# Kernel optimization log

Hardware: AMD Instinct MI355X
Metric: run time of the kernel (lower is better)

Reference implementation:

```python
import jax, jax.numpy as jnp
import numpy as np
from jax import lax

WS = 5      # window_size
NH = 8      # num_heads
C = 192     # channels
CPH = (2 * C // 3) // (2 * NH)  # per-head channel dim = 8


def _l2n(x):
    # F.normalize(dim=-1) with eps clamp
    n = jnp.linalg.norm(x, axis=-1, keepdims=True)
    return x / jnp.maximum(n, 1e-12)


def _conv3(x, w, b):
    y = lax.conv_general_dilated(x, w, (1, 1), 'SAME',
                                 dimension_numbers=('NCHW', 'OIHW', 'NCHW'))
    return y + b[None, :, None, None]


def _cpb_bias(cpb_w1, cpb_b1, cpb_w2):
    # relative coords table, Swin-V2 style log-spaced
    rel = np.arange(-(WS - 1), WS, dtype=np.float32)
    tbl = np.stack(np.meshgrid(rel, rel, indexing='ij'), axis=-1)  # (2W-1,2W-1,2)
    tbl = tbl / (WS - 1) * 8.0
    tbl = np.sign(tbl) * np.log2(np.abs(tbl) + 1.0) / np.log2(8.0)
    tbl = jnp.asarray(tbl.reshape(-1, 2))                          # (81,2)
    # relative position index (static int table)
    coords = np.stack(np.meshgrid(np.arange(WS), np.arange(WS), indexing='ij')).reshape(2, -1)
    rc = (coords[:, :, None] - coords[:, None, :]).transpose(1, 2, 0)  # (25,25,2)
    rc[..., 0] += WS - 1
    rc[..., 1] += WS - 1
    rc[..., 0] *= 2 * WS - 1
    idx = rc.sum(-1).reshape(-1)                                    # (625,)
    # cpb MLP: Linear(2,512)+ReLU, Linear(512,NH,no bias)
    h = jax.nn.relu(tbl @ cpb_w1.T + cpb_b1)
    bias_tbl = h @ cpb_w2.T                                         # (81, NH)
    bias = bias_tbl[idx].reshape(WS * WS, WS * WS, NH).transpose(2, 0, 1)
    return 16.0 * jax.nn.sigmoid(bias)                              # (NH,25,25)


def _wa(x, logit_scale, bias):
    # windowed cosine attention; note: scores are K@K^T (faithful to source)
    b, c2, h, w = x.shape
    hb, wb = h // WS, w // WS
    # 'b (kv head c) (h dh) (w dw) -> kv (b h w) head (dh dw) c'
    xr = x.reshape(b, 2, NH, CPH, hb, WS, wb, WS)
    xr = xr.transpose(1, 0, 4, 6, 2, 5, 7, 3).reshape(2, b * hb * wb, NH, WS * WS, CPH)
    k, v = xr[0], xr[1]
    kn = _l2n(k)
    scale = jnp.exp(jnp.minimum(logit_scale, jnp.log(100.0)))       # (NH,1,1)
    atn = jnp.einsum('wnic,wnjc->wnij', kn, kn) * scale + bias[None]
    atn = jax.nn.softmax(atn, axis=-1)
    y = jnp.einsum('wnij,wnjc->wnic', atn, v)                       # (bhw,NH,25,CPH)
    y = y.reshape(b, hb, wb, NH, WS, WS, CPH)
    y = y.transpose(0, 3, 6, 1, 4, 2, 5).reshape(b, NH * CPH, h, w)
    return y


def _forward(x, w_in, b_in, w_out, b_out, logit_scale, lr_logit_scale,
             cpb_w1, cpb_b1, cpb_w2):
    b, c, h, w = x.shape
    xp = _conv3(x, w_in, b_in)                                      # (b, 2c, h, w)
    ch = 2 * c // 3
    x0, x1, x2 = xp[:, :ch], xp[:, ch:2 * ch], xp[:, 2 * ch:]
    bias = _cpb_bias(cpb_w1, cpb_b1, cpb_w2)
    ys = []
    # branch 0: plain window attention
    ys.append(_wa(x0, logit_scale, bias))
    # branch 1: shifted windows (note asymmetric shifts, faithful to torch code)
    x1s = jnp.roll(x1, shift=(-WS // 2, -WS // 2), axis=(2, 3))
    y1 = _wa(x1s, logit_scale, bias)
    y1 = jnp.roll(y1, shift=(WS // 2, WS // 2), axis=(2, 3))
    ys.append(y1)
    # branch 2: long-range axial cosine attention
    xr = x2.reshape(b, 2, NH, CPH, h, w).transpose(1, 0, 4, 2, 5, 3)
    xr = xr.reshape(2, b * h, NH, w, CPH)                           # kv,(b h),head,w,c
    k, v = xr[0], xr[1]
    scale = jnp.exp(jnp.minimum(lr_logit_scale, jnp.log(100.0)))
    kn = _l2n(k)
    atn = jax.nn.softmax(jnp.einsum('bnic,bnjc->bnij', kn, kn) * scale, axis=-1)
    v = jnp.einsum('bnij,bnjc->bnic', atn, v)
    # '(b h) head w c -> (b w) head h c'
    k = k.reshape(b, h, NH, w, CPH).transpose(0, 3, 2, 1, 4).reshape(b * w, NH, h, CPH)
    v = v.reshape(b, h, NH, w, CPH).transpose(0, 3, 2, 1, 4).reshape(b * w, NH, h, CPH)
    kn = _l2n(k)
    atn = jax.nn.softmax(jnp.einsum('bnic,bnjc->bnij', kn, kn) * scale, axis=-1)
    v = jnp.einsum('bnij,bnjc->bnic', atn, v)
    # '(b w) head h c -> b (head c) h w'
    y2 = v.reshape(b, w, NH, h, CPH).transpose(0, 2, 4, 3, 1).reshape(b, NH * CPH, h, w)
    ys.append(y2)
    y = jnp.concatenate(ys, axis=1)                                 # (b, c, h, w)
    return _conv3(y, w_out, b_out)


def setup_inputs() -> dict:
    key = jax.random.key(0)
    ks = jax.random.split(key, 8)
    B, H, W = 2, 160, 160
    s = 0.02
    return {
        'x': jax.random.normal(ks[0], (B, C, H, W), jnp.float32),
        'w_in': jax.random.normal(ks[1], (2 * C, C, 3, 3), jnp.float32) * s,
        'b_in': jnp.zeros((2 * C,), jnp.float32),
        'w_out': jax.random.normal(ks[2], (C, C, 3, 3), jnp.float32) * s,
        'b_out': jnp.zeros((C,), jnp.float32),
        'logit_scale': jnp.log(10.0 * jnp.ones((NH, 1, 1), jnp.float32)),
        'lr_logit_scale': jnp.log(10.0 * jnp.ones((NH, 1, 1), jnp.float32)),
        'cpb_w1': jax.random.normal(ks[3], (512, 2), jnp.float32) * s,
        'cpb_b1': jnp.zeros((512,), jnp.float32),
        'cpb_w2': jax.random.normal(ks[4], (NH, 512), jnp.float32) * s,
    }


def reference(x, w_in, b_in, w_out, b_out, logit_scale, lr_logit_scale,
              cpb_w1, cpb_b1, cpb_w2):
    return _forward(x, w_in, b_in, w_out, b_out, logit_scale, lr_logit_scale,
                    cpb_w1, cpb_b1, cpb_w2)
```

## Files before the change

kernel.cpp:

```cpp
#include <hip/hip_runtime.h>
#include <math.h>


typedef __attribute__((ext_vector_type(8))) short short8;
typedef __attribute__((ext_vector_type(4))) short short4v;
typedef __attribute__((ext_vector_type(4))) float f32x4;

constexpr int Hc = 160, Wc = 160, Bc = 2;
constexpr int HPR = 162;
constexpr int HPW = 164;

__device__ inline unsigned short f2bf(float f) {
  union { float f; unsigned u; } v; v.f = f;
  unsigned r = v.u + 0x7FFF + ((v.u >> 16) & 1);
  return (unsigned short)(r >> 16);
}
__device__ inline float bf2f(unsigned short h) {
  union { unsigned u; float f; } v; v.u = ((unsigned)h) << 16;
  return v.f;
}

__device__ inline void gl16(const void* g, void* l) {
  __builtin_amdgcn_global_load_lds((const __attribute__((address_space(1))) unsigned int*)g,
                                   (__attribute__((address_space(3))) unsigned int*)l, 16, 0, 0);
}

__device__ inline float dot8(f32x4 a0, f32x4 a1, f32x4 b0, f32x4 b1) {
  float d = a0[0] * b0[0];
  d = fmaf(a0[1], b0[1], d); d = fmaf(a0[2], b0[2], d); d = fmaf(a0[3], b0[3], d);
  d = fmaf(a1[0], b1[0], d); d = fmaf(a1[1], b1[1], d);
  d = fmaf(a1[2], b1[2], d); d = fmaf(a1[3], b1[3], d);
  return d;
}

__global__ __launch_bounds__(256)
void prep_kernel(const float* __restrict__ x, unsigned short* __restrict__ xpad,
                 unsigned short* __restrict__ ypad,
                 const float* __restrict__ w_in, unsigned short* __restrict__ wtr1,
                 const float* __restrict__ w_out, unsigned short* __restrict__ wtr2,
                 const float* __restrict__ cw1, const float* __restrict__ cb1,
                 const float* __restrict__ cw2, float* __restrict__ biasf) {
  __shared__ float tile[192][33];
  const int bid = blockIdx.x;
  const int t = threadIdx.x;
  if (bid < 1600) {
    int blk = bid;
    const int w0 = (blk % 5) * 32; blk /= 5;
    const int h = blk % 160;
    const int b = blk / 160;
    for (int i = t; i < 192 * 32; i += 256) {
      int c = i >> 5, w = i & 31;
      tile[c][w] = x[(((size_t)b * 192 + c) * 160 + h) * 160 + w0 + w];
    }
    __syncthreads();
    for (int i = t; i < 32 * 192; i += 256) {
      int w = i / 192, c = i % 192;
      xpad[(((size_t)b * HPR + h + 1) * HPW + w0 + w + 1) * 192 + c] = f2bf(tile[c][w]);
    }
  } else if (bid < 1963) {
    const int NPOS = 968;
    const int total = 2 * 2 * NPOS * 24;
    int idx = (bid - 1600) * 256 + t;
    if (idx >= total) return;
    const int ch = idx % 24; int q = idx / 24;
    const int pos = q % NPOS; q /= NPOS;
    const int b = q & 1; const int buf = q >> 1;
    int row, col;
    if (pos < 328) { row = (pos < 164) ? 0 : 161; col = pos % 164; }
    else { int r = pos - 328; row = 1 + (r >> 2); int cm = r & 3; col = cm == 0 ? 0 : 160 + cm; }
    unsigned short* p = (buf ? ypad : xpad) + (((size_t)b * HPR + row) * HPW + col) * 192 + ch * 8;
    short8 z = {};
    *(short8*)p = z;
  } else if (bid < 2395) {
    const bool first = bid < 2251;
    const int CO = first ? 384 : 192;
    const int NT = CO / 16;
    const float* w = first ? w_in : w_out;
    unsigned short* wtr = first ? wtr1 : wtr2;
    int id = (bid - (first ? 1963 : 2251)) * 256 + t;
    if (id >= CO * 192) return;
    const int co = id / 192, ci = id % 192;
    const int cs = ci >> 5, kh = (ci >> 3) & 3, j = ci & 7;
    const int cotile = co >> 4, cor = co & 15;
    const float* wp = w + (size_t)id * 9;
#pragma unroll
    for (int tap = 0; tap < 9; ++tap)
      wtr[((((size_t)tap * 6 + cs) * NT + cotile) * 64 + kh * 16 + cor) * 8 + j] = f2bf(wp[tap]);
  } else {
    if (t >= 64) return;
    const int e = bid - 2395;
    const int d0 = e / 9, d1 = e % 9;
    const int r0 = d0 - 4, r1 = d1 - 4;
    float t0 = log2f(fabsf((float)r0) * 2.0f + 1.0f) * (1.0f / 3.0f); if (r0 < 0) t0 = -t0;
    float t1 = log2f(fabsf((float)r1) * 2.0f + 1.0f) * (1.0f / 3.0f); if (r1 < 0) t1 = -t1;
    const int lane = t;
    float acc[8];
#pragma unroll
    for (int n = 0; n < 8; ++n) acc[n] = 0.f;
    for (int k = lane; k < 512; k += 64) {
      float hk = fmaf(t0, cw1[k * 2 + 0], fmaf(t1, cw1[k * 2 + 1], cb1[k]));
      hk = fmaxf(hk, 0.f);
#pragma unroll
      for (int n = 0; n < 8; ++n) acc[n] = fmaf(hk, cw2[n * 512 + k], acc[n]);
    }
#pragma unroll
    for (int n = 0; n < 8; ++n) {
#pragma unroll
      for (int off = 32; off > 0; off >>= 1) acc[n] += __shfl_xor(acc[n], off, 64);
    }
    if (lane == 0) {
#pragma unroll
      for (int n = 0; n < 8; ++n)
        biasf[e * 8 + n] = 16.0f / (1.0f + expf(-acc[n]));
    }
  }
}

template<int COUT, int CT, int OUTMODE>
__global__ __launch_bounds__(256, 2)
void conv_mfma(const unsigned short* __restrict__ xin, const unsigned short* __restrict__ wtrA,
               const float* __restrict__ bias, unsigned short* __restrict__ obf,
               unsigned short* __restrict__ xk2k, unsigned short* __restrict__ xk2v,
               float* __restrict__ of32) {
  constexpr int CIN = 192;
  constexpr int R = 6;
  constexpr int TOTAL = R * 84 * 4;
  constexpr int SLAB = R * 84 * 32;
  constexpr int NT = COUT / 16;
  __shared__ unsigned short slab[2 * SLAB];
  const int t = threadIdx.x, lane = t & 63, wid = t >> 6;
  const int bx = blockIdx.x, cog = blockIdx.y, b = blockIdx.z;
  const int ws = bx & 1, hb = bx >> 1;
  const int w0 = ws * 80, h0 = hb * 4;
  const int hr = wid;
  const int l15 = lane & 15, l4 = lane >> 4;
  const int co0 = cog * (CT * 16);

  f32x4 acc[5][CT];
#pragma unroll
  for (int ct = 0; ct < CT; ++ct) {
    f32x4 bi;
#pragma unroll
    for (int r = 0; r < 4; ++r) bi[r] = bias[co0 + ct * 16 + l4 * 4 + r];
#pragma unroll
    for (int mt = 0; mt < 5; ++mt) acc[mt][ct] = bi;
  }

  auto stage = [&](int cs, int bufbase) {
#pragma unroll
    for (int ib0 = 0; ib0 < 8; ++ib0) {
      const int ib = ib0 * 4 + wid;
      const int n = ib * 64 + lane;
      if (n < TOTAL) {
        const int c = n & 3, q = n >> 2;
        const int r = q / 84, wv = q - r * 84;
        const int csrc = c ^ ((wv >> 1) & 3);
        const unsigned short* g = xin +
            (((size_t)b * HPR + h0 + r) * HPW + w0 + wv) * CIN + cs * 32 + csrc * 8;
        gl16(g, &slab[bufbase + ib * 512]);
      }
    }
  };

#define BARRIER_CNT                                                              \
  {                                                                              \
    if constexpr (CT == 4)                                                       \
      asm volatile("s_waitcnt vmcnt(36)\n\ts_barrier" ::: "memory");             \
    else                                                                         \
      asm volatile("s_waitcnt vmcnt(18)\n\ts_barrier" ::: "memory");             \
  }

#define LOADA(a, ky, cs)                                                         \
  {                                                                              \
    _Pragma("unroll")                                                            \
    for (int kx = 0; kx < 3; ++kx) {                                             \
      _Pragma("unroll")                                                          \
      for (int ct = 0; ct < CT; ++ct)                                            \
        a[kx * CT + ct] = *(const short8*)(wtrA +                                \
            ((size_t)(((ky) * 3 + kx) * 6 + (cs)) * NT + cog * CT + ct) * 512 +  \
            lane * 8);                                                           \
    }                                                                            \
  }

#define GROUP(a, ky, bufbase)                                                    \
  {                                                                              \
    const unsigned short* srow = &slab[(bufbase) + (hr + (ky)) * 84 * 32];       \
    _Pragma("unroll")                                                            \
    for (int kx = 0; kx < 3; ++kx) {                                             \
      _Pragma("unroll")                                                          \
      for (int mt = 0; mt < 5; ++mt) {                                           \
        const int wv = mt * 16 + l15 + kx;                                       \
        const int cr = l4 ^ ((wv >> 1) & 3);                                     \
        short8 bf = *(const short8*)(srow + wv * 32 + cr * 8);                   \
        _Pragma("unroll")                                                        \
        for (int ct = 0; ct < CT; ++ct)                                          \
          acc[mt][ct] =                                                          \
              __builtin_amdgcn_mfma_f32_16x16x32_bf16(a[kx * CT + ct], bf,       \
                                                      acc[mt][ct], 0, 0, 0);     \
      }                                                                          \
    }                                                                            \
  }

#define CSBODY(cs, base, nbase, LAST)                                            \
  {                                                                              \
    if (!(LAST)) stage((cs) + 1, nbase);                                         \
    __builtin_amdgcn_s_setprio(1);                                               \
    GROUP(A0f, 0, base);                                                         \
    __builtin_amdgcn_s_setprio(0);                                               \
    if (!(LAST)) LOADA(A0f, 0, (cs) + 1);                                        \
    __builtin_amdgcn_s_setprio(1);                                               \
    GROUP(A1f, 1, base);                                                         \
    __builtin_amdgcn_s_setprio(0);                                               \
    if (!(LAST)) LOADA(A1f, 1, (cs) + 1);                                        \
    __builtin_amdgcn_s_setprio(1);                                               \
    GROUP(A2f, 2, base);                                                         \
    __builtin_amdgcn_s_setprio(0);                                               \
    if (!(LAST)) {                                                               \
      LOADA(A2f, 2, (cs) + 1);                                                   \
      BARRIER_CNT;                                                               \
    }                                                                            \
  }

  short8 A0f[3 * CT], A1f[3 * CT], A2f[3 * CT];
  stage(0, 0);
  LOADA(A0f, 0, 0);
  LOADA(A1f, 1, 0);
  LOADA(A2f, 2, 0);
  BARRIER_CNT;

  CSBODY(0, 0, SLAB, 0);
  CSBODY(1, SLAB, 0, 0);
  CSBODY(2, 0, SLAB, 0);
  CSBODY(3, SLAB, 0, 0);
  CSBODY(4, 0, SLAB, 0);
  CSBODY(5, SLAB, 0, 1);
#undef LOADA
#undef GROUP
#undef CSBODY
#undef BARRIER_CNT

  const int h = h0 + hr;
  if (OUTMODE == 0) {
    if (co0 < 256) {
#pragma unroll
      for (int mt = 0; mt < 5; ++mt) {
        const int w = w0 + mt * 16 + l15;
        unsigned short* dst0 = obf + (((size_t)b * Hc + h) * Wc + w) * 256 + co0 + l4 * 4;
#pragma unroll
        for (int ct = 0; ct < CT; ++ct) {
          short4v s;
#pragma unroll
          for (int r = 0; r < 4; ++r) s[r] = (short)f2bf(acc[mt][ct][r]);
          *(short4v*)(dst0 + ct * 16) = s;
        }
      }
    } else {
      unsigned short* xk2 = (co0 == 256) ? xk2k : xk2v;
#pragma unroll
      for (int mt = 0; mt < 5; ++mt) {
        const int w = w0 + mt * 16 + l15;
#pragma unroll
        for (int ct = 0; ct < CT; ++ct) {
          const int rel = ct * 16 + l4 * 4;
          const int head = rel >> 3, within = rel & 7;
          short4v s;
#pragma unroll
          for (int r = 0; r < 4; ++r) s[r] = (short)f2bf(acc[mt][ct][r]);
          *(short4v*)(xk2 + ((((size_t)b * 8 + head) * 160 + h) * 160 + w) * 8 + within) = s;
        }
      }
    }
  } else {
#pragma unroll
    for (int mt = 0; mt < 5; ++mt) {
      const int w = w0 + mt * 16 + l15;
#pragma unroll
      for (int ct = 0; ct < CT; ++ct)
#pragma unroll
        for (int r = 0; r < 4; ++r) {
          const int co = co0 + ct * 16 + l4 * 4 + r;
          of32[(((size_t)b * COUT + co) * Hc + h) * Wc + w] = acc[mt][ct][r];
        }
    }
  }
}

__global__ __launch_bounds__(256)
void attn1_kernel(const unsigned short* __restrict__ xq, const float* __restrict__ biasf,
                  const float* __restrict__ logit_scale, const float* __restrict__ lrs,
                  const unsigned short* __restrict__ xk2k, const unsigned short* __restrict__ xk2v,
                  unsigned short* __restrict__ ypad, unsigned short* __restrict__ vrow) {
  const int bid = blockIdx.x;
  if (bid < 4096) {
    __shared__ f32x4 kn4[8][25][2];
    __shared__ f32x4 vv4[8][25][2];
    const int t = threadIdx.x;
    const int head = t & 7;
    const int i = t >> 3;
    const int b = bid >> 11;
    const int r = bid & 2047;
    const int variant = r >> 10;
    const int blk = r & 1023;
    const int chan_off = variant ? 128 : 0;
    const int y_ch_off = variant ? 64 : 0;
    const int shift_in = variant ? 3 : 0;
    const int shift_out = variant ? 2 : 0;
    const int wb_i = blk % 32, hb_i = blk / 32;
    const int wi = i / 5, wj = i % 5;
    const int gh = hb_i * 5 + wi, gw = wb_i * 5 + wj;
    const int sh = (gh + shift_in) % Hc, sw = (gw + shift_in) % Wc;

    if (i < 25) {
      const unsigned short* base = xq + (((size_t)b * Hc + sh) * Wc + sw) * 256 + chan_off + head * 8;
      short8 kv = *(const short8*)base;
      short8 vv = *(const short8*)(base + 64);
      float k[8]; float nrm = 0.f;
#pragma unroll
      for (int c = 0; c < 8; ++c) { k[c] = bf2f((unsigned short)kv[c]); nrm = fmaf(k[c], k[c], nrm); }
      const float inv = 1.0f / fmaxf(sqrtf(nrm), 1e-12f);
      f32x4 a0, a1, b0, b1;
#pragma unroll
      for (int c = 0; c < 4; ++c) { a0[c] = k[c] * inv; a1[c] = k[c + 4] * inv; }
#pragma unroll
      for (int c = 0; c < 4; ++c) { b0[c] = bf2f((unsigned short)vv[c]); b1[c] = bf2f((unsigned short)vv[c + 4]); }
      kn4[head][i][0] = a0; kn4[head][i][1] = a1;
      vv4[head][i][0] = b0; vv4[head][i][1] = b1;
    }
    __syncthreads();
    if (i >= 25) return;

    const float scale = expf(fminf(logit_scale[head], 4.6051702f));
    const f32x4 q0 = kn4[head][i][0], q1 = kn4[head][i][1];
    float s[25];
#pragma unroll
    for (int j = 0; j < 25; ++j) {
      const float d = dot8(q0, q1, kn4[head][j][0], kn4[head][j][1]);
      const int d0 = wi - (j / 5) + 4, d1 = wj - (j % 5) + 4;
      s[j] = fmaf(d, scale, biasf[(d0 * 9 + d1) * 8 + head]);
    }
    float m = -1e30f;
#pragma unroll
    for (int j = 0; j < 25; ++j) m = fmaxf(m, s[j]);
    float den = 0.f;
    f32x4 acc0 = {0.f, 0.f, 0.f, 0.f}, acc1 = {0.f, 0.f, 0.f, 0.f};
#pragma unroll
    for (int j = 0; j < 25; ++j) {
      const float p = __expf(s[j] - m);
      den += p;
      acc0 += vv4[head][j][0] * p;
      acc1 += vv4[head][j][1] * p;
    }
    const float rden = 1.0f / den;
    const int oh = (gh + shift_out) % Hc, ow = (gw + shift_out) % Wc;
    short8 o;
#pragma unroll
    for (int c = 0; c < 4; ++c) { o[c] = (short)f2bf(acc0[c] * rden); o[c + 4] = (short)f2bf(acc1[c] * rden); }
    *(short8*)(ypad + (((size_t)b * HPR + oh + 1) * HPW + ow + 1) * 192 + y_ch_off + head * 8) = o;
  } else {
    __shared__ f32x4 kn4[160][2];
    __shared__ f32x4 vv4[160][2];
    int u = bid - 4096;
    const int head = u % 8; u /= 8;
    const int h = u % 160;
    const int b = u / 160;
    const int i = threadIdx.x;

    if (i < 160) {
      const size_t base = ((((size_t)b * 8 + head) * 160 + h) * 160 + i) * 8;
      short8 kv = *(const short8*)(xk2k + base);
      short8 vv = *(const short8*)(xk2v + base);
      float k[8]; float nrm = 0.f;
#pragma unroll
      for (int c = 0; c < 8; ++c) { k[c] = bf2f((unsigned short)kv[c]); nrm = fmaf(k[c], k[c], nrm); }
      const float inv = 1.0f / fmaxf(sqrtf(nrm), 1e-12f);
      f32x4 a0, a1, b0, b1;
#pragma unroll
      for (int c = 0; c < 4; ++c) { a0[c] = k[c] * inv; a1[c] = k[c + 4] * inv; }
#pragma unroll
      for (int c = 0; c < 4; ++c) { b0[c] = bf2f((unsigned short)vv[c]); b1[c] = bf2f((unsigned short)vv[c + 4]); }
      kn4[i][0] = a0; kn4[i][1] = a1;
      vv4[i][0] = b0; vv4[i][1] = b1;
    }
    __syncthreads();
    if (i >= 160) return;

    const float scale = expf(fminf(lrs[head], 4.6051702f));
    const f32x4 q0 = kn4[i][0], q1 = kn4[i][1];
    float den = 0.f;
    f32x4 acc0 = {0.f, 0.f, 0.f, 0.f}, acc1 = {0.f, 0.f, 0.f, 0.f};
    for (int j = 0; j < 160; ++j) {
      const float d = dot8(q0, q1, kn4[j][0], kn4[j][1]);
      const float p = __expf(fmaf(d, scale, -scale));
      den += p;
      acc0 += vv4[j][0] * p;
      acc1 += vv4[j][1] * p;
    }
    const float rden = 1.0f / den;
    short8 o;
#pragma unroll
    for (int c = 0; c < 4; ++c) { o[c] = (short)f2bf(acc0[c] * rden); o[c + 4] = (short)f2bf(acc1[c] * rden); }
    *(short8*)(vrow + ((((size_t)b * 8 + head) * 160 + h) * 160 + i) * 8) = o;
  }
}

__global__ __launch_bounds__(640)
void col_attn_kernel(const unsigned short* __restrict__ xk2k, const float* __restrict__ lrs,
                     const unsigned short* __restrict__ vrow, unsigned short* __restrict__ ypad) {
  __shared__ f32x4 knT[4][161][2];
  __shared__ f32x4 vvT[4][161][2];
  int blk = blockIdx.x;
  const int wg = blk % 40; blk /= 40;
  const int head = blk % 8;
  const int b = blk / 8;
  const int w0 = wg * 4;
  const int t = threadIdx.x;

  {
    const int h = t >> 2, wc = t & 3;
    const size_t base = ((((size_t)b * 8 + head) * 160 + h) * 160 + (w0 + wc)) * 8;
    short8 kv = *(const short8*)(xk2k + base);
    short8 vv = *(const short8*)(vrow + base);
    float k[8]; float nrm = 0.f;
#pragma unroll
    for (int c = 0; c < 8; ++c) { k[c] = bf2f((unsigned short)kv[c]); nrm = fmaf(k[c], k[c], nrm); }
    const float inv = 1.0f / fmaxf(sqrtf(nrm), 1e-12f);
    f32x4 a0, a1, b0, b1;
#pragma unroll
    for (int c = 0; c < 4; ++c) { a0[c] = k[c] * inv; a1[c] = k[c + 4] * inv; }
#pragma unroll
    for (int c = 0; c < 4; ++c) { b0[c] = bf2f((unsigned short)vv[c]); b1[c] = bf2f((unsigned short)vv[c + 4]); }
    knT[wc][h][0] = a0; knT[wc][h][1] = a1;
    vvT[wc][h][0] = b0; vvT[wc][h][1] = b1;
  }
  __syncthreads();

  const int wi = t / 160, i = t % 160;
  const float scale = expf(fminf(lrs[head], 4.6051702f));
  const f32x4 q0 = knT[wi][i][0], q1 = knT[wi][i][1];
  float den = 0.f;
  f32x4 acc0 = {0.f, 0.f, 0.f, 0.f}, acc1 = {0.f, 0.f, 0.f, 0.f};
  for (int j = 0; j < 160; ++j) {
    const float d = dot8(q0, q1, knT[wi][j][0], knT[wi][j][1]);
    const float p = __expf(fmaf(d, scale, -scale));
    den += p;
    acc0 += vvT[wi][j][0] * p;
    acc1 += vvT[wi][j][1] * p;
  }
  const float rden = 1.0f / den;
  short8 o;
#pragma unroll
  for (int c = 0; c < 4; ++c) { o[c] = (short)f2bf(acc0[c] * rden); o[c + 4] = (short)f2bf(acc1[c] * rden); }
  *(short8*)(ypad + (((size_t)b * HPR + i + 1) * HPW + w0 + wi + 1) * 192 + 128 + head * 8) = o;
}

extern "C" void kernel_launch(void* const* d_in, const int* in_sizes, int n_in,
                              void* d_out, int out_size, void* d_ws, size_t ws_size,
                              hipStream_t stream) {
  const float* x     = (const float*)d_in[0];
  const float* w_in  = (const float*)d_in[1];
  const float* b_in  = (const float*)d_in[2];
  const float* w_out = (const float*)d_in[3];
  const float* b_out = (const float*)d_in[4];
  const float* ls    = (const float*)d_in[5];
  const float* lrs   = (const float*)d_in[6];
  const float* cw1   = (const float*)d_in[7];
  const float* cb1   = (const float*)d_in[8];
  const float* cw2   = (const float*)d_in[9];
  float* out = (float*)d_out;

  char* p = (char*)d_ws;
  unsigned short* xpad = (unsigned short*)p;  p += (size_t)Bc * HPR * HPW * 192 * 2;
  unsigned short* ypad = (unsigned short*)p;  p += (size_t)Bc * HPR * HPW * 192 * 2;
  unsigned short* xq   = (unsigned short*)p;  p += (size_t)Bc * Hc * Wc * 256 * 2;
  unsigned short* xk2k = (unsigned short*)p;  p += (size_t)Bc * 8 * Hc * Wc * 8 * 2;
  unsigned short* xk2v = (unsigned short*)p;  p += (size_t)Bc * 8 * Hc * Wc * 8 * 2;
  unsigned short* vrow = (unsigned short*)p;  p += (size_t)Bc * 8 * Hc * Wc * 8 * 2;
  unsigned short* wtr1 = (unsigned short*)p;  p += (size_t)9 * 384 * 192 * 2;
  unsigned short* wtr2 = (unsigned short*)p;  p += (size_t)9 * 192 * 192 * 2;
  float* biasf = (float*)p;

  prep_kernel<<<2476, 256, 0, stream>>>(x, xpad, ypad, w_in, wtr1, w_out, wtr2, cw1, cb1, cw2, biasf);
  conv_mfma<384, 4, 0><<<dim3(80, 6, Bc), 256, 0, stream>>>(xpad, wtr1, b_in, xq, xk2k, xk2v, nullptr);
  attn1_kernel<<<4096 + Bc * 160 * 8, 256, 0, stream>>>(xq, biasf, ls, lrs, xk2k, xk2v, ypad, vrow);
  col_attn_kernel<<<Bc * 8 * 40, 640, 0, stream>>>(xk2k, lrs, vrow, ypad);
  conv_mfma<192, 2, 1><<<dim3(80, 6, Bc), 256, 0, stream>>>(ypad, wtr2, b_out, nullptr, nullptr, nullptr, out);
}
```

Baseline: 235.6 us.

## Split output conv over input channels with atomic accumulation; vectorize xpad stores

The output conv grid doubles along z, and each block handles half of the input-channel slices (3 of 6). Partial sums are combined with float atomicAdd into an output that prep_kernel now zeroes first. Only the first half adds the bias. The aim is to raise occupancy and parallelism for the small 192-channel output conv, paid for with atomics, a zeroing pass over the output, and non-deterministic summation order. Separately, the prep transpose now writes 8 bf16 channels per store.

```diff
diff --git a/kernel.cpp b/kernel.cpp
--- a/kernel.cpp
+++ b/kernel.cpp
@@ -39,7 +39,8 @@
                  const float* __restrict__ w_in, unsigned short* __restrict__ wtr1,
                  const float* __restrict__ w_out, unsigned short* __restrict__ wtr2,
                  const float* __restrict__ cw1, const float* __restrict__ cb1,
-                 const float* __restrict__ cw2, float* __restrict__ biasf) {
+                 const float* __restrict__ cw2, float* __restrict__ biasf,
+                 float* __restrict__ outz) {
   __shared__ float tile[192][33];
   const int bid = blockIdx.x;
   const int t = threadIdx.x;
@@ -53,9 +54,12 @@
       tile[c][w] = x[(((size_t)b * 192 + c) * 160 + h) * 160 + w0 + w];
     }
     __syncthreads();
-    for (int i = t; i < 32 * 192; i += 256) {
-      int w = i / 192, c = i % 192;
-      xpad[(((size_t)b * HPR + h + 1) * HPW + w0 + w + 1) * 192 + c] = f2bf(tile[c][w]);
+    for (int i = t; i < 32 * 24; i += 256) {
+      int w = i / 24, c8 = i % 24;
+      short8 o;
+#pragma unroll
+      for (int k = 0; k < 8; ++k) o[k] = (short)f2bf(tile[c8 * 8 + k][w]);
+      *(short8*)(xpad + (((size_t)b * HPR + h + 1) * HPW + w0 + w + 1) * 192 + c8 * 8) = o;
     }
   } else if (bid < 1963) {
     const int NPOS = 968;
@@ -86,7 +90,7 @@
 #pragma unroll
     for (int tap = 0; tap < 9; ++tap)
       wtr[((((size_t)tap * 6 + cs) * NT + cotile) * 64 + kh * 16 + cor) * 8 + j] = f2bf(wp[tap]);
-  } else {
+  } else if (bid < 2476) {
     if (t >= 64) return;
     const int e = bid - 2395;
     const int d0 = e / 9, d1 = e % 9;
@@ -112,6 +116,12 @@
 #pragma unroll
       for (int n = 0; n < 8; ++n)
         biasf[e * 8 + n] = 16.0f / (1.0f + expf(-acc[n]));
+    }
+  } else {
+    const long chunk = (long)(bid - 2476) * 256 + t;
+    if (chunk < 2457600) {
+      f32x4 z = {0.f, 0.f, 0.f, 0.f};
+      *(f32x4*)(outz + chunk * 4) = z;
     }
   }
 }
@@ -129,7 +139,11 @@
   constexpr int NT = COUT / 16;
   __shared__ unsigned short slab[2 * SLAB];
   const int t = threadIdx.x, lane = t & 63, wid = t >> 6;
-  const int bx = blockIdx.x, cog = blockIdx.y, b = blockIdx.z;
+  const int bx = blockIdx.x, cog = blockIdx.y;
+  const int zz = blockIdx.z;
+  const int b    = (OUTMODE == 2) ? (zz >> 1) : zz;
+  const int half = (OUTMODE == 2) ? (zz & 1) : 0;
+  const int cs0  = half * 3;
   const int ws = bx & 1, hb = bx >> 1;
   const int w0 = ws * 80, h0 = hb * 4;
   const int hr = wid;
@@ -141,7 +155,8 @@
   for (int ct = 0; ct < CT; ++ct) {
     f32x4 bi;
 #pragma unroll
-    for (int r = 0; r < 4; ++r) bi[r] = bias[co0 + ct * 16 + l4 * 4 + r];
+    for (int r = 0; r < 4; ++r)
+      bi[r] = (OUTMODE == 2 && half != 0) ? 0.f : bias[co0 + ct * 16 + l4 * 4 + r];
 #pragma unroll
     for (int mt = 0; mt < 5; ++mt) acc[mt][ct] = bi;
   }
@@ -222,18 +237,24 @@
   }
 
   short8 A0f[3 * CT], A1f[3 * CT], A2f[3 * CT];
-  stage(0, 0);
-  LOADA(A0f, 0, 0);
-  LOADA(A1f, 1, 0);
-  LOADA(A2f, 2, 0);
+  stage(cs0, 0);
+  LOADA(A0f, 0, cs0);
+  LOADA(A1f, 1, cs0);
+  LOADA(A2f, 2, cs0);
   BARRIER_CNT;
 
-  CSBODY(0, 0, SLAB, 0);
-  CSBODY(1, SLAB, 0, 0);
-  CSBODY(2, 0, SLAB, 0);
-  CSBODY(3, SLAB, 0, 0);
-  CSBODY(4, 0, SLAB, 0);
-  CSBODY(5, SLAB, 0, 1);
+  if constexpr (OUTMODE == 2) {
+    CSBODY(cs0 + 0, 0, SLAB, 0);
+    CSBODY(cs0 + 1, SLAB, 0, 0);
+    CSBODY(cs0 + 2, 0, SLAB, 1);
+  } else {
+    CSBODY(0, 0, SLAB, 0);
+    CSBODY(1, SLAB, 0, 0);
+    CSBODY(2, 0, SLAB, 0);
+    CSBODY(3, SLAB, 0, 0);
+    CSBODY(4, 0, SLAB, 0);
+    CSBODY(5, SLAB, 0, 1);
+  }
 #undef LOADA
 #undef GROUP
 #undef CSBODY
@@ -270,7 +291,7 @@
         }
       }
     }
-  } else {
+  } else if (OUTMODE == 1) {
 #pragma unroll
     for (int mt = 0; mt < 5; ++mt) {
       const int w = w0 + mt * 16 + l15;
@@ -280,6 +301,18 @@
         for (int r = 0; r < 4; ++r) {
           const int co = co0 + ct * 16 + l4 * 4 + r;
           of32[(((size_t)b * COUT + co) * Hc + h) * Wc + w] = acc[mt][ct][r];
+        }
+    }
+  } else {
+#pragma unroll
+    for (int mt = 0; mt < 5; ++mt) {
+      const int w = w0 + mt * 16 + l15;
+#pragma unroll
+      for (int ct = 0; ct < CT; ++ct)
+#pragma unroll
+        for (int r = 0; r < 4; ++r) {
+          const int co = co0 + ct * 16 + l4 * 4 + r;
+          atomicAdd(&of32[(((size_t)b * COUT + co) * Hc + h) * Wc + w], acc[mt][ct][r]);
         }
     }
   }
@@ -479,9 +512,10 @@
   unsigned short* wtr2 = (unsigned short*)p;  p += (size_t)9 * 192 * 192 * 2;
   float* biasf = (float*)p;
 
-  prep_kernel<<<2476, 256, 0, stream>>>(x, xpad, ypad, w_in, wtr1, w_out, wtr2, cw1, cb1, cw2, biasf);
+  prep_kernel<<<12076, 256, 0, stream>>>(x, xpad, ypad, w_in, wtr1, w_out, wtr2,
+                                         cw1, cb1, cw2, biasf, out);
   conv_mfma<384, 4, 0><<<dim3(80, 6, Bc), 256, 0, stream>>>(xpad, wtr1, b_in, xq, xk2k, xk2v, nullptr);
   attn1_kernel<<<4096 + Bc * 160 * 8, 256, 0, stream>>>(xq, biasf, ls, lrs, xk2k, xk2v, ypad, vrow);
   col_attn_kernel<<<Bc * 8 * 40, 640, 0, stream>>>(xk2k, lrs, vrow, ypad);
-  conv_mfma<192, 2, 1><<<dim3(80, 6, Bc), 256, 0, stream>>>(ypad, wtr2, b_out, nullptr, nullptr, nullptr, out);
-}
+  conv_mfma<192, 2, 2><<<dim3(80, 6, Bc * 2), 256, 0, stream>>>(ypad, wtr2, b_out, nullptr, nullptr, nullptr, out);
+}
```

New measurement: 276.4 us. 1.17x slower.

## Split conv output channels across two wave groups per block and vectorize xpad pack

Applied to the files above, without the earlier changes.

The MFMA conv kernel now runs 512-thread blocks in which pairs of waves share one input slab but each computes half of the block's output-channel tile. This halves per-wave accumulator count, lowering register pressure and raising occupancy, and it lets the second conv use half as many blocks while keeping the same channel coverage per block. The staging loop is regeneralized for eight waves, and the k/v scatter indexing is adjusted for the new channel offsets. Separately, the prep kernel's transpose-to-bf16 writes now store eight channels per 16-byte write instead of scalar stores. The BARRIER_CNT vmcnt constants were not updated for the new load counts per wave, which may make the waits overly conservative or wrong.

```diff
diff --git a/kernel.cpp b/kernel.cpp
--- a/kernel.cpp
+++ b/kernel.cpp
@@ -53,9 +53,12 @@
       tile[c][w] = x[(((size_t)b * 192 + c) * 160 + h) * 160 + w0 + w];
     }
     __syncthreads();
-    for (int i = t; i < 32 * 192; i += 256) {
-      int w = i / 192, c = i % 192;
-      xpad[(((size_t)b * HPR + h + 1) * HPW + w0 + w + 1) * 192 + c] = f2bf(tile[c][w]);
+    for (int i = t; i < 32 * 24; i += 256) {
+      int w = i / 24, c8 = i % 24;
+      short8 o;
+#pragma unroll
+      for (int k = 0; k < 8; ++k) o[k] = (short)f2bf(tile[c8 * 8 + k][w]);
+      *(short8*)(xpad + (((size_t)b * HPR + h + 1) * HPW + w0 + w + 1) * 192 + c8 * 8) = o;
     }
   } else if (bid < 1963) {
     const int NPOS = 968;
@@ -116,25 +119,27 @@
   }
 }
 
-template<int COUT, int CT, int OUTMODE>
-__global__ __launch_bounds__(256, 2)
+template<int COUT, int CT, int NWH, int OUTMODE>
+__global__ __launch_bounds__(256 * NWH, 4)
 void conv_mfma(const unsigned short* __restrict__ xin, const unsigned short* __restrict__ wtrA,
                const float* __restrict__ bias, unsigned short* __restrict__ obf,
                unsigned short* __restrict__ xk2k, unsigned short* __restrict__ xk2v,
                float* __restrict__ of32) {
   constexpr int CIN = 192;
   constexpr int R = 6;
+  constexpr int WAVES = 4 * NWH;
   constexpr int TOTAL = R * 84 * 4;
   constexpr int SLAB = R * 84 * 32;
   constexpr int NT = COUT / 16;
+  constexpr int IB0 = (TOTAL / 64 + WAVES - 1) / WAVES;
   __shared__ unsigned short slab[2 * SLAB];
   const int t = threadIdx.x, lane = t & 63, wid = t >> 6;
   const int bx = blockIdx.x, cog = blockIdx.y, b = blockIdx.z;
   const int ws = bx & 1, hb = bx >> 1;
   const int w0 = ws * 80, h0 = hb * 4;
-  const int hr = wid;
+  const int hr = wid / NWH, wh = wid % NWH;
   const int l15 = lane & 15, l4 = lane >> 4;
-  const int co0 = cog * (CT * 16);
+  const int co0 = cog * (CT * 16 * NWH) + wh * (CT * 16);
 
   f32x4 acc[5][CT];
 #pragma unroll
@@ -148,8 +153,8 @@
 
   auto stage = [&](int cs, int bufbase) {
 #pragma unroll
-    for (int ib0 = 0; ib0 < 8; ++ib0) {
-      const int ib = ib0 * 4 + wid;
+    for (int ib0 = 0; ib0 < IB0; ++ib0) {
+      const int ib = ib0 * WAVES + wid;
       const int n = ib * 64 + lane;
       if (n < TOTAL) {
         const int c = n & 3, q = n >> 2;
@@ -177,8 +182,8 @@
       _Pragma("unroll")                                                          \
       for (int ct = 0; ct < CT; ++ct)                                            \
         a[kx * CT + ct] = *(const short8*)(wtrA +                                \
-            ((size_t)(((ky) * 3 + kx) * 6 + (cs)) * NT + cog * CT + ct) * 512 +  \
-            lane * 8);                                                           \
+            ((size_t)(((ky) * 3 + kx) * 6 + (cs)) * NT + cog * (CT * NWH) +      \
+             wh * CT + ct) * 512 + lane * 8);                                    \
     }                                                                            \
   }
 
@@ -255,13 +260,14 @@
         }
       }
     } else {
-      unsigned short* xk2 = (co0 == 256) ? xk2k : xk2v;
+      unsigned short* xk2 = (co0 < 320) ? xk2k : xk2v;
+      const int cb = co0 & 63;
 #pragma unroll
       for (int mt = 0; mt < 5; ++mt) {
         const int w = w0 + mt * 16 + l15;
 #pragma unroll
         for (int ct = 0; ct < CT; ++ct) {
-          const int rel = ct * 16 + l4 * 4;
+          const int rel = cb + ct * 16 + l4 * 4;
           const int head = rel >> 3, within = rel & 7;
           short4v s;
 #pragma unroll
@@ -480,8 +486,8 @@
   float* biasf = (float*)p;
 
   prep_kernel<<<2476, 256, 0, stream>>>(x, xpad, ypad, w_in, wtr1, w_out, wtr2, cw1, cb1, cw2, biasf);
-  conv_mfma<384, 4, 0><<<dim3(80, 6, Bc), 256, 0, stream>>>(xpad, wtr1, b_in, xq, xk2k, xk2v, nullptr);
+  conv_mfma<384, 2, 2, 0><<<dim3(80, 6, Bc), 512, 0, stream>>>(xpad, wtr1, b_in, xq, xk2k, xk2v, nullptr);
   attn1_kernel<<<4096 + Bc * 160 * 8, 256, 0, stream>>>(xq, biasf, ls, lrs, xk2k, xk2v, ypad, vrow);
   col_attn_kernel<<<Bc * 8 * 40, 640, 0, stream>>>(xk2k, lrs, vrow, ypad);
-  conv_mfma<192, 2, 1><<<dim3(80, 6, Bc), 256, 0, stream>>>(ypad, wtr2, b_out, nullptr, nullptr, nullptr, out);
-}
+  conv_mfma<192, 2, 2, 1><<<dim3(80, 3, Bc), 512, 0, stream>>>(ypad, wtr2, b_out, nullptr, nullptr, nullptr, out);
+}
```

New measurement: 246.8 us. +4.7%, slower.
